# Kernel tuning notes

Hardware: AMD Instinct MI355X
Metric: run time of the kernel (lower is better)

Reference implementation:

```python
import jax, jax.numpy as jnp
import numpy as np

# ---- grid / table constants (Deep Marching Cubes style; tables synthesized deterministically) ----
W = H = D = 40          # cells per axis -> N = 64000 cells
T = 256                 # marching-cubes topologies
NCFG = 96               # topology configs that carry triangles
MAXT = 4                # max triangles per config
N = W * H * D

_rs = np.random.RandomState(0)
TOPO2TRI = _rs.randint(0, T, size=NCFG)                       # config -> topology column
TRI_EDGES = _rs.rand(NCFG, MAXT, 12).argsort(-1)[..., :3]      # [NCFG,MAXT,3] distinct cell-edge ids
_NTRI = _rs.randint(1, MAXT + 1, size=NCFG)
TRI_MASK = (np.arange(MAXT)[None, :] < _NTRI[:, None]).astype(np.float32)   # [NCFG,MAXT]
PAIR_MASK = jnp.asarray(TRI_MASK[:, :-1] * TRI_MASK[:, 1:])                 # [NCFG,MAXT-1]

# 12 cell edges: (dx,dy,dz of base corner, axis of edge)
EDGES = [(0,0,0,0),(0,1,0,0),(0,0,1,0),(0,1,1,0),
         (0,0,0,1),(1,0,0,1),(0,0,1,1),(1,0,1,1),
         (0,0,0,2),(1,0,0,2),(0,1,0,2),(1,1,0,2)]
BASE = np.stack(np.meshgrid(np.arange(W), np.arange(H), np.arange(D), indexing='ij'), -1).astype(np.float32)  # [W,H,D,3]
AXIS = np.eye(3, dtype=np.float32)
E0 = jnp.asarray(TRI_EDGES[..., 0]); E1 = jnp.asarray(TRI_EDGES[..., 1]); E2 = jnp.asarray(TRI_EDGES[..., 2])
TOPO2TRI_J = jnp.asarray(TOPO2TRI)


def _edge_vertices(off):
    """off: [3, W+1, H+1, D+1] -> per-cell edge intersection vertices [N, 12, 3]."""
    verts = []
    for dx, dy, dz, ax in EDGES:
        o = off[ax, dx:dx + W, dy:dy + H, dz:dz + D]                 # [W,H,D]
        corner = jnp.asarray(np.array([dx, dy, dz], dtype=np.float32))
        pos = (jnp.asarray(BASE) + corner) + o[..., None] * jnp.asarray(AXIS[ax])  # [W,H,D,3]
        verts.append(pos)
    return jnp.stack(verts, axis=3).reshape(N, 12, 3)


def _curvature_loss(off, topo):
    v = _edge_vertices(off)                         # [N,12,3]
    p0 = v[:, E0]                                   # [N,NCFG,MAXT,3]
    d1 = v[:, E1] - p0
    d2 = v[:, E2] - p0
    n = jnp.cross(d1, d2)                           # triangle normals
    n = n / (jnp.linalg.norm(n, axis=-1, keepdims=True) + 1e-8)
    cosang = jnp.sum(n[:, :, :-1] * n[:, :, 1:], axis=-1)          # [N,NCFG,MAXT-1]
    curv = jnp.sum((1.0 - cosang) * PAIR_MASK, axis=-1)            # [N,NCFG]
    return jnp.sum(topo[:, TOPO2TRI_J] * curv)                     # scalar curvature loss


def setup_inputs() -> dict:
    key = jax.random.key(0)
    k1, k2 = jax.random.split(key)
    off = 0.3 * jax.random.normal(k1, (3, W + 1, H + 1, D + 1), dtype=jnp.float32)
    topo = jax.random.uniform(k2, (N, T), dtype=jnp.float32)
    return {"off": off, "topo": topo}


def reference(off, topo):
    return _curvature_loss(off, topo)
```

## Files before the change

### kernel.cpp

```cpp
#include <hip/hip_runtime.h>
#include <stdint.h>

#define NCFG 96
#define NSUB 4
#define NBLK 1000
#define NPART NBLK

namespace ct {

struct Tabs {
  int topo2tri[NCFG];
  int e0[NCFG][4];
  int e1[NCFG][4];
  int e2[NCFG][4];
  int ntri[NCFG];
  int nactive;
  int aorder[NCFG];
};

struct MT {
  uint32_t mt[624];
  int pos;
  constexpr MT() : mt{}, pos(624) {
    uint32_t s = 0u;
    for (int i = 0; i < 624; ++i) {
      mt[i] = s;
      s = 1812433253u * (s ^ (s >> 30)) + (uint32_t)(i + 1);
    }
  }
  constexpr uint32_t next() {
    if (pos >= 624) {
      for (int i = 0; i < 624; ++i) {
        uint32_t y = (mt[i] & 0x80000000u) |
                     (mt[(i + 1) == 624 ? 0 : (i + 1)] & 0x7fffffffu);
        uint32_t v = mt[(i + 397) >= 624 ? (i + 397 - 624) : (i + 397)] ^ (y >> 1);
        if (y & 1u) v ^= 0x9908b0dfu;
        mt[i] = v;
      }
      pos = 0;
    }
    uint32_t y = mt[pos++];
    y ^= y >> 11;
    y ^= (y << 7) & 0x9d2c5680u;
    y ^= (y << 15) & 0xefc60000u;
    y ^= y >> 18;
    return y;
  }
};

constexpr Tabs make_tabs() {
  Tabs t{};
  MT g{};
  for (int i = 0; i < NCFG; ++i) t.topo2tri[i] = (int)(g.next() & 255u);
  for (int c = 0; c < NCFG; ++c) {
    for (int tr = 0; tr < 4; ++tr) {
      uint64_t key[12] = {};
      for (int k = 0; k < 12; ++k) {
        uint64_t a = (uint64_t)(g.next() >> 5);
        uint64_t b = (uint64_t)(g.next() >> 6);
        key[k] = (a << 26) | b;
      }
      bool used[12] = {};
      int sel[3] = {};
      for (int s = 0; s < 3; ++s) {
        int best = -1;
        for (int k = 0; k < 12; ++k)
          if (!used[k] && (best < 0 || key[k] < key[best])) best = k;
        used[best] = true;
        sel[s] = best;
      }
      t.e0[c][tr] = sel[0];
      t.e1[c][tr] = sel[1];
      t.e2[c][tr] = sel[2];
    }
  }
  for (int c = 0; c < NCFG; ++c) t.ntri[c] = 1 + (int)(g.next() & 3u);
  int na = 0;
  for (int i = 0; i < NCFG; ++i)
    if (t.ntri[i] > 1) t.aorder[na++] = i;
  t.nactive = na;
  for (int i = 1; i < na; ++i) {
    int v = t.aorder[i];
    int j = i - 1;
    while (j >= 0 && t.topo2tri[t.aorder[j]] > t.topo2tri[v]) {
      t.aorder[j + 1] = t.aorder[j];
      --j;
    }
    t.aorder[j + 1] = v;
  }
  return t;
}

constexpr Tabs TAB = make_tabs();

constexpr int EDX[12] = {0,0,0,0, 0,1,0,1, 0,1,0,1};
constexpr int EDY[12] = {0,1,0,1, 0,0,0,0, 0,0,1,1};
constexpr int EDZ[12] = {0,0,1,1, 0,0,1,1, 0,0,0,0};
constexpr int EAX[12] = {0,0,0,0, 1,1,1,1, 2,2,2,2};

constexpr int NA = TAB.nactive;
constexpr int SPLIT(int k) { return k * NA / NSUB; }

}


template<int C, int T>
__device__ __forceinline__ void tri_nq(const float (&o)[12], float (&n)[3], float& q) {
  constexpr int ea = ct::TAB.e0[C][T];
  constexpr int eb = ct::TAB.e1[C][T];
  constexpr int ec = ct::TAB.e2[C][T];
  float d1[3] = { (float)(ct::EDX[eb] - ct::EDX[ea]),
                  (float)(ct::EDY[eb] - ct::EDY[ea]),
                  (float)(ct::EDZ[eb] - ct::EDZ[ea]) };
  float d2[3] = { (float)(ct::EDX[ec] - ct::EDX[ea]),
                  (float)(ct::EDY[ec] - ct::EDY[ea]),
                  (float)(ct::EDZ[ec] - ct::EDZ[ea]) };
  d1[ct::EAX[eb]] += o[eb];
  d1[ct::EAX[ea]] -= o[ea];
  d2[ct::EAX[ec]] += o[ec];
  d2[ct::EAX[ea]] -= o[ea];
  n[0] = d1[1] * d2[2] - d1[2] * d2[1];
  n[1] = d1[2] * d2[0] - d1[0] * d2[2];
  n[2] = d1[0] * d2[1] - d1[1] * d2[0];
  q = n[0]*n[0] + n[1]*n[1] + n[2]*n[2];
}

__device__ __forceinline__ float pair_term(const float (&a)[3], float qa,
                                           const float (&b)[3], float qb) {
  float d = a[0]*b[0] + a[1]*b[1] + a[2]*b[2];
  return 1.0f - d * __builtin_amdgcn_rsqf(qa * qb);
}

template<int C>
__device__ __forceinline__ float config_curv(const float (&o)[12]) {
  constexpr int NT = ct::TAB.ntri[C];
  float n0[3], n1[3], n2[3], n3[3];
  float q0 = 0.f, q1 = 0.f, q2 = 0.f, q3 = 0.f;
  tri_nq<C, 0>(o, n0, q0);
  tri_nq<C, 1>(o, n1, q1);
  if constexpr (NT > 2) tri_nq<C, 2>(o, n2, q2);
  if constexpr (NT > 3) tri_nq<C, 3>(o, n3, q3);
  float curv = pair_term(n0, q0, n1, q1);
  if constexpr (NT > 2) curv += pair_term(n1, q1, n2, q2);
  if constexpr (NT > 3) curv += pair_term(n2, q2, n3, q3);
  return curv;
}

template<int I, int END>
__device__ __forceinline__ void do_act(const float (&o)[12],
                                       const float* __restrict__ topoRow,
                                       float& acc, float carry) {
  if constexpr (I < END) {
    constexpr int c   = ct::TAB.aorder[I];
    constexpr int col = ct::TAB.topo2tri[c];
    float nc = carry + config_curv<c>(o);
    constexpr bool flush = (I + 1 == END) ||
        (ct::TAB.topo2tri[ct::TAB.aorder[(I + 1 < END) ? I + 1 : I]] != col);
    if constexpr (flush) {
      acc += topoRow[col] * nc;
      do_act<I + 1, END>(o, topoRow, acc, 0.0f);
    } else {
      do_act<I + 1, END>(o, topoRow, acc, nc);
    }
  }
}

__global__ __launch_bounds__(256)
void curv_kernel(const float* __restrict__ off, const float* __restrict__ topo,
                 float* __restrict__ partials) {
  const int lane = threadIdx.x & 63;
  const int w    = threadIdx.x >> 6;
  const int cell = blockIdx.x * 64 + lane;
  const int x = cell / 1600;
  const int r = cell - x * 1600;
  const int y = r / 40;
  const int z = r - y * 40;

  float o[12];
#pragma unroll
  for (int e = 0; e < 12; ++e) {
    o[e] = off[ct::EAX[e] * 68921 + (x + ct::EDX[e]) * 1681 +
               (y + ct::EDY[e]) * 41 + (z + ct::EDZ[e])];
  }

  const float* topoRow = topo + (size_t)cell * 256;
  float acc = 0.0f;
  switch (w) {
    case 0:  do_act<ct::SPLIT(0), ct::SPLIT(1)>(o, topoRow, acc, 0.0f); break;
    case 1:  do_act<ct::SPLIT(1), ct::SPLIT(2)>(o, topoRow, acc, 0.0f); break;
    case 2:  do_act<ct::SPLIT(2), ct::SPLIT(3)>(o, topoRow, acc, 0.0f); break;
    default: do_act<ct::SPLIT(3), ct::SPLIT(4)>(o, topoRow, acc, 0.0f); break;
  }

#pragma unroll
  for (int d = 32; d > 0; d >>= 1) acc += __shfl_down(acc, d, 64);
  __shared__ float wsum[4];
  if (lane == 0) wsum[w] = acc;
  __syncthreads();
  if (threadIdx.x == 0)
    partials[blockIdx.x] = wsum[0] + wsum[1] + wsum[2] + wsum[3];
}

__global__ __launch_bounds__(256)
void reduce_kernel(const float* __restrict__ partials, float* __restrict__ out) {
  float s = 0.0f;
  for (int i = threadIdx.x; i < NPART; i += 256) s += partials[i];
#pragma unroll
  for (int d = 32; d > 0; d >>= 1) s += __shfl_down(s, d, 64);
  __shared__ float wsum[4];
  const int lane = threadIdx.x & 63;
  const int w = threadIdx.x >> 6;
  if (lane == 0) wsum[w] = s;
  __syncthreads();
  if (threadIdx.x == 0) out[0] = wsum[0] + wsum[1] + wsum[2] + wsum[3];
}

extern "C" void kernel_launch(void* const* d_in, const int* in_sizes, int n_in,
                              void* d_out, int out_size, void* d_ws, size_t ws_size,
                              hipStream_t stream) {
  const float* off  = (const float*)d_in[0];
  const float* topo = (const float*)d_in[1];
  float* out = (float*)d_out;
  float* partials = (float*)d_ws;

  curv_kernel<<<dim3(NBLK), dim3(256), 0, stream>>>(off, topo, partials);
  reduce_kernel<<<dim3(1), dim3(256), 0, stream>>>(partials, out);
}
```

Baseline: 21.11 us.

## Stage per-cell curvature coefficients in LDS and read topo rows coalesced

Instead of each thread gathering scattered topo columns from its own 1 KB row, every wave now reads 16 full topo rows with coalesced float4 loads, issued up front so they overlap the curvature math. Per-cell, per-column curvature coefficients go into a zero-initialised, padded LDS tile and are then dotted with the topo registers. The wave split points are moved so that no topology column spans two waves, which avoids write conflicts. The cost is reading the whole 64 MB topo array instead of only the needed columns (which may already touch most cache lines), plus about 66 KB of LDS per block and two extra barriers, which lowers occupancy.

```diff
diff --git a/kernel.cpp b/kernel.cpp
--- a/kernel.cpp
+++ b/kernel.cpp
@@ -5,6 +5,8 @@
 #define NSUB 4
 #define NBLK 1000
 #define NPART NBLK
+#define CSTRIDE 260
+#define CFLOATS (64 * CSTRIDE)
 
 namespace ct {
 
@@ -99,7 +101,16 @@
 constexpr int EAX[12] = {0,0,0,0, 1,1,1,1, 2,2,2,2};
 
 constexpr int NA = TAB.nactive;
-constexpr int SPLIT(int k) { return k * NA / NSUB; }
+
+constexpr int snap(int s) {
+  int r = s;
+  while (r > 0 && r < NA &&
+         TAB.topo2tri[TAB.aorder[r - 1]] == TAB.topo2tri[TAB.aorder[r]]) ++r;
+  return r;
+}
+constexpr int SPLIT(int k) {
+  return (k <= 0) ? 0 : (k >= NSUB ? NA : snap(k * NA / NSUB));
+}
 
 }
 
@@ -147,9 +158,8 @@
 }
 
 template<int I, int END>
-__device__ __forceinline__ void do_act(const float (&o)[12],
-                                       const float* __restrict__ topoRow,
-                                       float& acc, float carry) {
+__device__ __forceinline__ void do_coef(const float (&o)[12],
+                                        float* __restrict__ ldsRow, float carry) {
   if constexpr (I < END) {
     constexpr int c   = ct::TAB.aorder[I];
     constexpr int col = ct::TAB.topo2tri[c];
@@ -157,10 +167,10 @@
     constexpr bool flush = (I + 1 == END) ||
         (ct::TAB.topo2tri[ct::TAB.aorder[(I + 1 < END) ? I + 1 : I]] != col);
     if constexpr (flush) {
-      acc += topoRow[col] * nc;
-      do_act<I + 1, END>(o, topoRow, acc, 0.0f);
+      ldsRow[col] = nc;
+      do_coef<I + 1, END>(o, ldsRow, 0.0f);
     } else {
-      do_act<I + 1, END>(o, topoRow, acc, nc);
+      do_coef<I + 1, END>(o, ldsRow, nc);
     }
   }
 }
@@ -168,14 +178,24 @@
 __global__ __launch_bounds__(256)
 void curv_kernel(const float* __restrict__ off, const float* __restrict__ topo,
                  float* __restrict__ partials) {
-  const int lane = threadIdx.x & 63;
-  const int w    = threadIdx.x >> 6;
+  __shared__ __align__(16) float coef[CFLOATS];
+  const int tid  = (int)threadIdx.x;
+  const int lane = tid & 63;
+  const int w    = tid >> 6;
+
+  float4 t[16];
+  {
+    const float* tp = topo + (size_t)(blockIdx.x * 64 + w * 16) * 256 + lane * 4;
+#pragma unroll
+    for (int k = 0; k < 16; ++k)
+      t[k] = *(const float4*)(tp + (size_t)k * 256);
+  }
+
   const int cell = blockIdx.x * 64 + lane;
   const int x = cell / 1600;
   const int r = cell - x * 1600;
   const int y = r / 40;
   const int z = r - y * 40;
-
   float o[12];
 #pragma unroll
   for (int e = 0; e < 12; ++e) {
@@ -183,13 +203,27 @@
                (y + ct::EDY[e]) * 41 + (z + ct::EDZ[e])];
   }
 
-  const float* topoRow = topo + (size_t)cell * 256;
+  {
+    const float4 zz = make_float4(0.f, 0.f, 0.f, 0.f);
+    for (int i = tid * 4; i < CFLOATS; i += 1024)
+      *(float4*)&coef[i] = zz;
+  }
+  __syncthreads();
+
+  float* ldsRow = &coef[lane * CSTRIDE];
+  switch (w) {
+    case 0:  do_coef<ct::SPLIT(0), ct::SPLIT(1)>(o, ldsRow, 0.0f); break;
+    case 1:  do_coef<ct::SPLIT(1), ct::SPLIT(2)>(o, ldsRow, 0.0f); break;
+    case 2:  do_coef<ct::SPLIT(2), ct::SPLIT(3)>(o, ldsRow, 0.0f); break;
+    default: do_coef<ct::SPLIT(3), ct::SPLIT(4)>(o, ldsRow, 0.0f); break;
+  }
+  __syncthreads();
+
   float acc = 0.0f;
-  switch (w) {
-    case 0:  do_act<ct::SPLIT(0), ct::SPLIT(1)>(o, topoRow, acc, 0.0f); break;
-    case 1:  do_act<ct::SPLIT(1), ct::SPLIT(2)>(o, topoRow, acc, 0.0f); break;
-    case 2:  do_act<ct::SPLIT(2), ct::SPLIT(3)>(o, topoRow, acc, 0.0f); break;
-    default: do_act<ct::SPLIT(3), ct::SPLIT(4)>(o, topoRow, acc, 0.0f); break;
+#pragma unroll
+  for (int k = 0; k < 16; ++k) {
+    const float4 cf = *(const float4*)&coef[(w * 16 + k) * CSTRIDE + lane * 4];
+    acc += t[k].x * cf.x + t[k].y * cf.y + t[k].z * cf.z + t[k].w * cf.w;
   }
 
 #pragma unroll
@@ -197,7 +231,7 @@
   __shared__ float wsum[4];
   if (lane == 0) wsum[w] = acc;
   __syncthreads();
-  if (threadIdx.x == 0)
+  if (tid == 0)
     partials[blockIdx.x] = wsum[0] + wsum[1] + wsum[2] + wsum[3];
 }
 
```

New measurement: 21.27 us. Within noise of the previous version (+0.8%).
